# Performance work log

Measured on AMD Instinct MI355X. Metric: run time of the kernel, lower is better.

Reference implementation:

```python
import jax, jax.numpy as jnp
import numpy as np

B, S, D = 4, 1024, 1024
H, HD = 16, 64  # num_heads, head_dim; H*HD == D (qkv_features)
NEG_BIG = -1e10


def setup_inputs() -> dict:
    key = jax.random.key(0)
    ks = jax.random.split(key, 16)
    inp = {
        'inputs_q': jax.random.normal(ks[0], (B, S, D), jnp.float32),
        'inputs_kv': jax.random.normal(ks[1], (B, S, D), jnp.float32),
        'pos_emb_q': jax.random.normal(ks[2], (B, S, D), jnp.float32),
        'pos_emb_k': jax.random.normal(ks[3], (B, S, D), jnp.float32),
        'pos_emb_v': jax.random.normal(ks[4], (B, S, D), jnp.float32),
        'key_padding_mask': jnp.ones((B, S), jnp.float32),
    }
    scale = 1.0 / np.sqrt(D)
    inp['wq'] = jax.random.normal(ks[5], (D, H, HD), jnp.float32) * scale
    inp['bq'] = jnp.zeros((H, HD), jnp.float32)
    inp['wk'] = jax.random.normal(ks[6], (D, H, HD), jnp.float32) * scale
    inp['bk'] = jnp.zeros((H, HD), jnp.float32)
    inp['wv'] = jax.random.normal(ks[7], (D, H, HD), jnp.float32) * scale
    inp['bv'] = jnp.zeros((H, HD), jnp.float32)
    inp['wo'] = jax.random.normal(ks[8], (H, HD, D), jnp.float32) * scale
    inp['bo'] = jnp.zeros((D,), jnp.float32)
    return inp


def reference(inputs_q, inputs_kv, pos_emb_q, pos_emb_k, pos_emb_v,
              key_padding_mask, wq, bq, wk, bk, wv, bv, wo, bo):
    # Add positional embeddings before QKV projections (DETR style).
    q_in = inputs_q + pos_emb_q
    k_in = inputs_kv + pos_emb_k
    v_in = inputs_kv + pos_emb_v
    # DenseGeneral: [b,s,f] x [f,h,d] -> [b,s,h,d]
    q = jnp.einsum('bsf,fhd->bshd', q_in, wq) + bq
    k = jnp.einsum('bsf,fhd->bshd', k_in, wk) + bk
    v = jnp.einsum('bsf,fhd->bshd', v_in, wv) + bv
    # Additive key-padding bias, broadcast to [b,1,1,kv].
    bias = ((1.0 - key_padding_mask) * NEG_BIG)[:, None, None, :]
    q = q / jnp.sqrt(jnp.asarray(HD, q.dtype))
    attn = jnp.einsum('bqhd,bkhd->bhqk', q, k) + bias
    attn = jax.nn.softmax(attn, axis=-1)
    # (train=False: no dropout; identity capture layer is a no-op.)
    x = jnp.einsum('bhqk,bkhd->bqhd', attn, v)
    # Output projection over (heads, head_dim).
    out = jnp.einsum('bqhd,hdf->bqf', x, wo) + bo
    return out
```

## Files before the change

### kernel.cpp

```cpp
#include <hip/hip_runtime.h>
#include <hip/hip_bf16.h>
#include <stdint.h>

typedef __bf16 bf16_t;
typedef __bf16 bf16x8 __attribute__((ext_vector_type(8)));
typedef __bf16 bf16x4v __attribute__((ext_vector_type(4)));
typedef float  f32x4  __attribute__((ext_vector_type(4)));
typedef float  f32x16 __attribute__((ext_vector_type(16)));
typedef unsigned int u32;
typedef u32 u32x4 __attribute__((ext_vector_type(4)));

#define NEG_BIG (-1e10f)
#define LOG2E 1.44269504f

__device__ __forceinline__ void load_lds16(const void* gsrc, void* ldst) {
  __builtin_amdgcn_global_load_lds(
      (__attribute__((address_space(1))) void*)(gsrc),
      (__attribute__((address_space(3))) void*)(ldst), 16, 0, 0);
}

__device__ __forceinline__ u32 cvt_pk_bf16(float lo, float hi) {
  u32 r;
  asm("v_cvt_pk_bf16_f32 %0, %1, %2" : "=v"(r) : "v"(lo), "v"(hi));
  return r;
}

__global__ __launch_bounds__(256) void k_prep_w(
    const float* __restrict__ iq, const float* __restrict__ ikv,
    const float* __restrict__ pq, const float* __restrict__ pk, const float* __restrict__ pv,
    const float* __restrict__ wq, const float* __restrict__ wk,
    const float* __restrict__ wv, const float* __restrict__ wo,
    bf16_t* __restrict__ Xq, bf16_t* __restrict__ Xk, bf16_t* __restrict__ Xv,
    bf16_t* __restrict__ Wt, bf16_t* __restrict__ Wot)
{
  __shared__ float t[64][65];
  if (blockIdx.x < 4096) {
    int i = blockIdx.x * 256 + threadIdx.x;
    float4 a = ((const float4*)iq)[i], b = ((const float4*)ikv)[i];
    float4 eq = ((const float4*)pq)[i], ek = ((const float4*)pk)[i], ev = ((const float4*)pv)[i];
    bf16x4v q, k, v;
    q[0] = (bf16_t)(a.x + eq.x); q[1] = (bf16_t)(a.y + eq.y);
    q[2] = (bf16_t)(a.z + eq.z); q[3] = (bf16_t)(a.w + eq.w);
    k[0] = (bf16_t)(b.x + ek.x); k[1] = (bf16_t)(b.y + ek.y);
    k[2] = (bf16_t)(b.z + ek.z); k[3] = (bf16_t)(b.w + ek.w);
    v[0] = (bf16_t)(b.x + ev.x); v[1] = (bf16_t)(b.y + ev.y);
    v[2] = (bf16_t)(b.z + ev.z); v[3] = (bf16_t)(b.w + ev.w);
    *(bf16x4v*)&Xq[(size_t)i*4] = q;
    *(bf16x4v*)&Xk[(size_t)i*4] = k;
    *(bf16x4v*)&Xv[(size_t)i*4] = v;
  } else {
    int bid = blockIdx.x - 4096;
    int z = bid >> 8, rem = bid & 255;
    const float* src = z==0 ? wq : z==1 ? wk : z==2 ? wv : wo;
    bf16_t*      dst = z < 3 ? (Wt + (size_t)z*(1u<<20)) : Wot;
    int n0 = (rem & 15) << 6, k0 = (rem >> 4) << 6;
    int c = threadIdx.x & 63, rb = threadIdx.x >> 6;
    #pragma unroll
    for (int i = 0; i < 16; ++i) {
      int r = i*4 + rb;
      t[r][c] = src[(size_t)(k0 + r)*1024 + n0 + c];
    }
    __syncthreads();
    #pragma unroll
    for (int i = 0; i < 16; ++i) {
      int r = i*4 + rb;
      dst[(size_t)(n0 + r)*1024 + k0 + c] = (bf16_t)t[c][r];
    }
  }
}

__global__ __launch_bounds__(256, 3) void k_gemm_qkv(
    const bf16_t* __restrict__ Xq, const bf16_t* __restrict__ Xk, const bf16_t* __restrict__ Xv,
    const bf16_t* __restrict__ Wt,
    const float* __restrict__ bq, const float* __restrict__ bk, const float* __restrict__ bv,
    bf16_t* __restrict__ Qo, bf16_t* __restrict__ Ko, bf16_t* __restrict__ Vt)
{
  const int L = blockIdx.x;
  const int w = (L & 7) * 96 + (L >> 3);
  const int bx = w & 7, by = (w >> 3) & 31, bz = w >> 8;
  const int bn = bz * 8 + bx;

  const bf16_t* A = bz==0 ? Xq : bz==1 ? Xk : Xv;
  const float* bias = bz==0 ? bq : bz==1 ? bk : bv;

  __shared__ bf16_t As[128*64];
  __shared__ bf16_t Bs[128*64];

  const int tid = threadIdx.x, lane = tid & 63, wid = tid >> 6;
  const int wm = wid >> 1, wn = wid & 1;
  const int bm0 = by * 128;
  const int bn0g = bn * 128;
  const int g = lane >> 4, c = lane & 15;
  const int sr = lane >> 3, sch = lane & 7;

  f32x4 acc[4][4] = {};

  #define STAGE(kt_)                                                             \
    { _Pragma("unroll")                                                          \
      for (int i = 0; i < 4; ++i) {                                              \
        int r  = wid*32 + i*8 + sr;                                              \
        int ca = sch ^ (r & 7);                                                  \
        load_lds16(A  + (size_t)(bm0  + r)*1024 + (size_t)(kt_)*64 + ca*8,       \
                   &As[(wid*32 + i*8)*64]);                                      \
        load_lds16(Wt + (size_t)(bn0g + r)*1024 + (size_t)(kt_)*64 + ca*8,       \
                   &Bs[(wid*32 + i*8)*64]);                                      \
      } }

  for (int kt = 0; kt < 16; ++kt) {
    STAGE(kt);
    __syncthreads();
    #pragma unroll
    for (int kk = 0; kk < 2; ++kk) {
      bf16x8 af[4], bfr[4];
      #pragma unroll
      for (int m = 0; m < 4; ++m) {
        int row = wm*64 + m*16 + c;
        int ch  = (kk*4 + g) ^ (row & 7);
        af[m] = *(const bf16x8*)&As[row*64 + ch*8];
      }
      #pragma unroll
      for (int n = 0; n < 4; ++n) {
        int row = wn*64 + n*16 + c;
        int ch  = (kk*4 + g) ^ (row & 7);
        bfr[n] = *(const bf16x8*)&Bs[row*64 + ch*8];
      }
      #pragma unroll
      for (int m = 0; m < 4; ++m)
        #pragma unroll
        for (int n = 0; n < 4; ++n)
          acc[m][n] = __builtin_amdgcn_mfma_f32_16x16x32_bf16(af[m], bfr[n], acc[m][n], 0, 0, 0);
    }
    __syncthreads();
  }
  #undef STAGE

  if (bz < 2) {
    bf16_t* C = bz==0 ? Qo : Ko;
    const float scale = bz==0 ? 0.125f * LOG2E : 1.0f;
    #pragma unroll
    for (int n = 0; n < 4; ++n) {
      int col = (bn0g & 1023) + wn*64 + n*16 + c;
      float bn_ = bias[col];
      #pragma unroll
      for (int m = 0; m < 4; ++m) {
        int row0 = bm0 + wm*64 + m*16 + g*4;
        #pragma unroll
        for (int r = 0; r < 4; ++r)
          C[(size_t)(row0 + r)*1024 + col] = (bf16_t)((acc[m][n][r] + bn_) * scale);
      }
    }
  } else {
    #pragma unroll
    for (int n = 0; n < 4; ++n) {
      int colz = (bn0g & 1023) + wn*64 + n*16 + c;
      float bn_ = bias[colz];
      int h = colz >> 6, hd = colz & 63;
      #pragma unroll
      for (int m = 0; m < 4; ++m) {
        int row0 = bm0 + wm*64 + m*16 + g*4;
        int b = row0 >> 10, s0 = row0 & 1023;
        bf16x4v v4;
        #pragma unroll
        for (int r = 0; r < 4; ++r) v4[r] = (bf16_t)(acc[m][n][r] + bn_);
        *(bf16x4v*)&Vt[(size_t)((b*16 + h)*64 + hd)*1024 + s0] = v4;
      }
    }
  }
}

__global__ __launch_bounds__(256, 2) void k_attn2(
    const bf16_t* __restrict__ Qm, const bf16_t* __restrict__ Km,
    const bf16_t* __restrict__ Vt, const float* __restrict__ mask,
    bf16_t* __restrict__ X2)
{
  __shared__ bf16_t Ks[2][64*64];
  __shared__ bf16_t Vs[2][64*64];
  __shared__ float  bias_lds[1024];
  __shared__ int    tflag[16];
  __shared__ float  l_lds[4][32];

  const int L = blockIdx.x;
  const int kk_ = L >> 3;
  const int bh = (L & 7) * 8 + (kk_ >> 3);
  const int qt = kk_ & 7;
  const int b = bh >> 4, h = bh & 15;

  const int tid = threadIdx.x, lane = tid & 63, wid = tid >> 6;
  const int lq = lane & 31;
  const int hi = lane >> 5;

  if (tid < 16) tflag[tid] = 0;
  __syncthreads();
  {
    float4 m4 = *(const float4*)&mask[b*1024 + tid*4];
    float4 b4;
    b4.x = (1.0f - m4.x) * (NEG_BIG * LOG2E);
    b4.y = (1.0f - m4.y) * (NEG_BIG * LOG2E);
    b4.z = (1.0f - m4.z) * (NEG_BIG * LOG2E);
    b4.w = (1.0f - m4.w) * (NEG_BIG * LOG2E);
    *(float4*)&bias_lds[tid*4] = b4;
    if (b4.x != 0.f || b4.y != 0.f || b4.z != 0.f || b4.w != 0.f)
      tflag[tid >> 4] = 1;
  }

  const int q0w = qt*128 + wid*32;
  bf16x8 qf[4];
  #pragma unroll
  for (int kb = 0; kb < 4; ++kb)
    qf[kb] = *(const bf16x8*)&Qm[(size_t)(b*1024 + q0w + lq)*1024 + h*64 + kb*16 + hi*8];

  f32x16 oacc[2] = {};
  float lsum = 0.f;

  const int sr8 = (lane >> 3);
  const int sc8 = lane & 7;
  #define STAGE(bufi, kv0)                                                        \
    {                                                                             \
      _Pragma("unroll")                                                           \
      for (int cc = 0; cc < 2; ++cc) {                                            \
        int r  = cc*32 + wid*8 + sr8;                                             \
        int ca = sc8 ^ (r & 7);                                                   \
        load_lds16(Km + (size_t)(b*1024 + (kv0) + r)*1024 + h*64 + ca*8,          \
                   &Ks[bufi][(cc*32 + wid*8)*64]);                                \
        load_lds16(Vt + (size_t)((b*16 + h)*64 + r)*1024 + (kv0) + ca*8,          \
                   &Vs[bufi][(cc*32 + wid*8)*64]);                                \
      }                                                                           \
    }

  STAGE(0, 0);
  __syncthreads();

  for (int kt = 0; kt < 16; ++kt) {
    const int buf = kt & 1;
    if (kt < 15) STAGE(buf ^ 1, (kt + 1) * 64);

    f32x16 s[2];
    __builtin_amdgcn_s_setprio(1);
    #pragma unroll
    for (int blk = 0; blk < 2; ++blk) {
      f32x16 acc = {};
      #pragma unroll
      for (int kb = 0; kb < 4; ++kb) {
        int row = blk*32 + lq;
        int ch  = (kb*2 + hi) ^ (row & 7);
        bf16x8 kf = *(const bf16x8*)&Ks[buf][row*64 + ch*8];
        acc = __builtin_amdgcn_mfma_f32_32x32x16_bf16(kf, qf[kb], acc, 0, 0, 0);
      }
      s[blk] = acc;
    }
    __builtin_amdgcn_s_setprio(0);

    if (tflag[kt]) {
      #pragma unroll
      for (int blk = 0; blk < 2; ++blk)
        #pragma unroll
        for (int g2 = 0; g2 < 4; ++g2) {
          float4 b4 = *(const float4*)&bias_lds[kt*64 + blk*32 + g2*8 + hi*4];
          s[blk][g2*4+0] += b4.x;
          s[blk][g2*4+1] += b4.y;
          s[blk][g2*4+2] += b4.z;
          s[blk][g2*4+3] += b4.w;
        }
    }

    #pragma unroll
    for (int blk = 0; blk < 2; ++blk)
      #pragma unroll
      for (int r = 0; r < 16; ++r) {
        float sv = fminf(s[blk][r], 60.0f);
        asm("v_exp_f32 %0, %1" : "=v"(sv) : "v"(sv));
        s[blk][r] = sv;
      }

    float ts[8];
    #pragma unroll
    for (int r = 0; r < 8; ++r)
      ts[r] = (s[0][r] + s[0][r+8]) + (s[1][r] + s[1][r+8]);
    float s0 = (ts[0] + ts[1]) + (ts[2] + ts[3]);
    float s1 = (ts[4] + ts[5]) + (ts[6] + ts[7]);
    float rsum = s0 + s1;
    lsum += rsum + __shfl_xor(rsum, 32, 64);

    u32 paw[4][4];
    #pragma unroll
    for (int blk = 0; blk < 2; ++blk)
      #pragma unroll
      for (int half = 0; half < 2; ++half) {
        int base = half * 8;
        #pragma unroll
        for (int w2 = 0; w2 < 2; ++w2) {
          u32 x = cvt_pk_bf16(s[blk][base + 2*w2],     s[blk][base + 2*w2 + 1]);
          u32 y = cvt_pk_bf16(s[blk][base + 4 + 2*w2], s[blk][base + 4 + 2*w2 + 1]);
          asm("v_permlane32_swap_b32 %0, %1" : "+v"(x), "+v"(y));
          paw[blk*2 + half][w2]     = x;
          paw[blk*2 + half][w2 + 2] = y;
        }
      }

    __builtin_amdgcn_s_setprio(1);
    #pragma unroll
    for (int ks = 0; ks < 4; ++ks) {
      u32x4 t = { paw[ks][0], paw[ks][1], paw[ks][2], paw[ks][3] };
      bf16x8 pa = __builtin_bit_cast(bf16x8, t);
      #pragma unroll
      for (int nb = 0; nb < 2; ++nb) {
        int row = nb*32 + lq;
        int ch  = (ks*2 + hi) ^ (row & 7);
        bf16x8 vf = *(const bf16x8*)&Vs[buf][row*64 + ch*8];
        oacc[nb] = __builtin_amdgcn_mfma_f32_32x32x16_bf16(pa, vf, oacc[nb], 0, 0, 0);
      }
    }
    __builtin_amdgcn_s_setprio(0);
    __syncthreads();
  }

  l_lds[wid][lq] = lsum;
  __syncthreads();
  #pragma unroll
  for (int g2 = 0; g2 < 4; ++g2)
    #pragma unroll
    for (int j = 0; j < 4; ++j) {
      int reg  = g2*4 + j;
      int qrow = j + 8*g2 + 4*hi;
      float inv = 1.0f / l_lds[wid][qrow];
      #pragma unroll
      for (int nb = 0; nb < 2; ++nb)
        X2[(size_t)(b*1024 + q0w + qrow)*1024 + h*64 + nb*32 + lq] =
            (bf16_t)(oacc[nb][reg] * inv);
    }
  #undef STAGE
}

__global__ __launch_bounds__(256, 3) void k_gemm_out(
    const bf16_t* __restrict__ A, const bf16_t* __restrict__ Bt,
    const float* __restrict__ bo, float* __restrict__ C)
{
  const int L = blockIdx.x;
  const int w = (L & 7) * 32 + (L >> 3);
  const int bx = w & 7, by = w >> 3;

  __shared__ bf16_t As[128*64];
  __shared__ bf16_t Bs[128*64];

  const int tid = threadIdx.x, lane = tid & 63, wid = tid >> 6;
  const int wm = wid >> 1, wn = wid & 1;
  const int bm0 = by * 128, bn0 = bx * 128;
  const int g = lane >> 4, c = lane & 15;
  const int sr = lane >> 3, sch = lane & 7;

  f32x4 acc[4][4] = {};

  #define STAGEO(kt_)                                                            \
    { _Pragma("unroll")                                                          \
      for (int i = 0; i < 4; ++i) {                                              \
        int r  = wid*32 + i*8 + sr;                                              \
        int ca = sch ^ (r & 7);                                                  \
        load_lds16(A  + (size_t)(bm0 + r)*1024 + (size_t)(kt_)*64 + ca*8,        \
                   &As[(wid*32 + i*8)*64]);                                      \
        load_lds16(Bt + (size_t)(bn0 + r)*1024 + (size_t)(kt_)*64 + ca*8,        \
                   &Bs[(wid*32 + i*8)*64]);                                      \
      } }

  for (int kt = 0; kt < 16; ++kt) {
    STAGEO(kt);
    __syncthreads();
    #pragma unroll
    for (int kk = 0; kk < 2; ++kk) {
      bf16x8 af[4], bfr[4];
      #pragma unroll
      for (int m = 0; m < 4; ++m) {
        int row = wm*64 + m*16 + c;
        int ch  = (kk*4 + g) ^ (row & 7);
        af[m] = *(const bf16x8*)&As[row*64 + ch*8];
      }
      #pragma unroll
      for (int n = 0; n < 4; ++n) {
        int row = wn*64 + n*16 + c;
        int ch  = (kk*4 + g) ^ (row & 7);
        bfr[n] = *(const bf16x8*)&Bs[row*64 + ch*8];
      }
      #pragma unroll
      for (int m = 0; m < 4; ++m)
        #pragma unroll
        for (int n = 0; n < 4; ++n)
          acc[m][n] = __builtin_amdgcn_mfma_f32_16x16x32_bf16(af[m], bfr[n], acc[m][n], 0, 0, 0);
    }
    __syncthreads();
  }
  #undef STAGEO

  #pragma unroll
  for (int n = 0; n < 4; ++n) {
    int col = bn0 + wn*64 + n*16 + c;
    float bn_ = bo[col];
    #pragma unroll
    for (int m = 0; m < 4; ++m) {
      int row0 = bm0 + wm*64 + m*16 + g*4;
      #pragma unroll
      for (int r = 0; r < 4; ++r)
        C[(size_t)(row0 + r)*1024 + col] = acc[m][n][r] + bn_;
    }
  }
}

extern "C" void kernel_launch(void* const* d_in, const int* in_sizes, int n_in,
                              void* d_out, int out_size, void* d_ws, size_t ws_size,
                              hipStream_t stream) {
  const float* iq   = (const float*)d_in[0];
  const float* ikv  = (const float*)d_in[1];
  const float* pq   = (const float*)d_in[2];
  const float* pk   = (const float*)d_in[3];
  const float* pv   = (const float*)d_in[4];
  const float* mask = (const float*)d_in[5];
  const float* wq   = (const float*)d_in[6];
  const float* bq   = (const float*)d_in[7];
  const float* wk   = (const float*)d_in[8];
  const float* bk   = (const float*)d_in[9];
  const float* wv   = (const float*)d_in[10];
  const float* bv   = (const float*)d_in[11];
  const float* wo   = (const float*)d_in[12];
  const float* bo   = (const float*)d_in[13];
  float* out = (float*)d_out;

  char* ws = (char*)d_ws;
  bf16_t* Xq  = (bf16_t*)(ws + (size_t)( 0u<<20));
  bf16_t* Xk  = (bf16_t*)(ws + (size_t)( 8u<<20));
  bf16_t* Xv  = (bf16_t*)(ws + (size_t)(16u<<20));
  bf16_t* Wt  = (bf16_t*)(ws + (size_t)(24u<<20));
  bf16_t* Wot = (bf16_t*)(ws + (size_t)(30u<<20));
  bf16_t* Q   = (bf16_t*)(ws + (size_t)(32u<<20));
  bf16_t* K   = (bf16_t*)(ws + (size_t)(40u<<20));
  bf16_t* Vt  = (bf16_t*)(ws + (size_t)(56u<<20));
  bf16_t* X2  = (bf16_t*)(ws + (size_t)(64u<<20));

  k_prep_w<<<5120, 256, 0, stream>>>(iq, ikv, pq, pk, pv, wq, wk, wv, wo,
                                     Xq, Xk, Xv, Wt, Wot);
  k_gemm_qkv<<<768, 256, 0, stream>>>(Xq, Xk, Xv, Wt, bq, bk, bv, Q, K, Vt);
  k_attn2<<<512, 256, 0, stream>>>(Q, K, Vt, mask, X2);
  k_gemm_out<<<256, 256, 0, stream>>>(X2, Wot, bo, out);
}
```

Baseline: 106.9 us.

## Split attention KV range across two wave groups per block with LDS reduction

The attention kernel now runs 512 threads per block, and two groups of four waves each process half of the key/value sequence for the same query tile. Partial outputs and row sums from the second half are reduced through LDS before normalisation and the store. The goal is more waves per CU and a shorter serial KV loop per wave, so latency is hidden better across the 512 blocks. The cost is doubled LDS for K/V buffers, an extra reduction step with barriers, and possibly lower block occupancy.

```diff
diff --git a/kernel.cpp b/kernel.cpp
--- a/kernel.cpp
+++ b/kernel.cpp
@@ -168,16 +168,17 @@
   }
 }
 
-__global__ __launch_bounds__(256, 2) void k_attn2(
+__global__ __launch_bounds__(512, 4) void k_attn2(
     const bf16_t* __restrict__ Qm, const bf16_t* __restrict__ Km,
     const bf16_t* __restrict__ Vt, const float* __restrict__ mask,
     bf16_t* __restrict__ X2)
 {
-  __shared__ bf16_t Ks[2][64*64];
-  __shared__ bf16_t Vs[2][64*64];
+  __shared__ bf16_t Ks[2][2][64*64];
+  __shared__ bf16_t Vs[2][2][64*64];
   __shared__ float  bias_lds[1024];
   __shared__ int    tflag[16];
   __shared__ float  l_lds[4][32];
+  __shared__ float  l2_lds[4][32];
 
   const int L = blockIdx.x;
   const int kk_ = L >> 3;
@@ -186,24 +187,23 @@
   const int b = bh >> 4, h = bh & 15;
 
   const int tid = threadIdx.x, lane = tid & 63, wid = tid >> 6;
+  const int half = wid >> 2, w4 = wid & 3;
   const int lq = lane & 31;
   const int hi = lane >> 5;
 
   if (tid < 16) tflag[tid] = 0;
   __syncthreads();
   {
-    float4 m4 = *(const float4*)&mask[b*1024 + tid*4];
-    float4 b4;
-    b4.x = (1.0f - m4.x) * (NEG_BIG * LOG2E);
-    b4.y = (1.0f - m4.y) * (NEG_BIG * LOG2E);
-    b4.z = (1.0f - m4.z) * (NEG_BIG * LOG2E);
-    b4.w = (1.0f - m4.w) * (NEG_BIG * LOG2E);
-    *(float4*)&bias_lds[tid*4] = b4;
-    if (b4.x != 0.f || b4.y != 0.f || b4.z != 0.f || b4.w != 0.f)
-      tflag[tid >> 4] = 1;
-  }
-
-  const int q0w = qt*128 + wid*32;
+    float2 m2 = *(const float2*)&mask[b*1024 + tid*2];
+    float2 b2;
+    b2.x = (1.0f - m2.x) * (NEG_BIG * LOG2E);
+    b2.y = (1.0f - m2.y) * (NEG_BIG * LOG2E);
+    *(float2*)&bias_lds[tid*2] = b2;
+    if (b2.x != 0.f || b2.y != 0.f)
+      tflag[tid >> 5] = 1;
+  }
+
+  const int q0w = qt*128 + w4*32;
   bf16x8 qf[4];
   #pragma unroll
   for (int kb = 0; kb < 4; ++kb)
@@ -218,21 +218,22 @@
     {                                                                             \
       _Pragma("unroll")                                                           \
       for (int cc = 0; cc < 2; ++cc) {                                            \
-        int r  = cc*32 + wid*8 + sr8;                                             \
+        int r  = cc*32 + w4*8 + sr8;                                              \
         int ca = sc8 ^ (r & 7);                                                   \
         load_lds16(Km + (size_t)(b*1024 + (kv0) + r)*1024 + h*64 + ca*8,          \
-                   &Ks[bufi][(cc*32 + wid*8)*64]);                                \
+                   &Ks[half][bufi][(cc*32 + w4*8)*64]);                           \
         load_lds16(Vt + (size_t)((b*16 + h)*64 + r)*1024 + (kv0) + ca*8,          \
-                   &Vs[bufi][(cc*32 + wid*8)*64]);                                \
+                   &Vs[half][bufi][(cc*32 + w4*8)*64]);                           \
       }                                                                           \
     }
 
-  STAGE(0, 0);
+  STAGE(0, half*512);
   __syncthreads();
 
-  for (int kt = 0; kt < 16; ++kt) {
-    const int buf = kt & 1;
-    if (kt < 15) STAGE(buf ^ 1, (kt + 1) * 64);
+  for (int t = 0; t < 8; ++t) {
+    const int kt = half*8 + t;
+    const int buf = t & 1;
+    if (t < 7) STAGE(buf ^ 1, (kt + 1) * 64);
 
     f32x16 s[2];
     __builtin_amdgcn_s_setprio(1);
@@ -243,7 +244,7 @@
       for (int kb = 0; kb < 4; ++kb) {
         int row = blk*32 + lq;
         int ch  = (kb*2 + hi) ^ (row & 7);
-        bf16x8 kf = *(const bf16x8*)&Ks[buf][row*64 + ch*8];
+        bf16x8 kf = *(const bf16x8*)&Ks[half][buf][row*64 + ch*8];
         acc = __builtin_amdgcn_mfma_f32_32x32x16_bf16(kf, qf[kb], acc, 0, 0, 0);
       }
       s[blk] = acc;
@@ -285,50 +286,66 @@
     #pragma unroll
     for (int blk = 0; blk < 2; ++blk)
       #pragma unroll
-      for (int half = 0; half < 2; ++half) {
-        int base = half * 8;
+      for (int hf = 0; hf < 2; ++hf) {
+        int base = hf * 8;
         #pragma unroll
         for (int w2 = 0; w2 < 2; ++w2) {
           u32 x = cvt_pk_bf16(s[blk][base + 2*w2],     s[blk][base + 2*w2 + 1]);
           u32 y = cvt_pk_bf16(s[blk][base + 4 + 2*w2], s[blk][base + 4 + 2*w2 + 1]);
           asm("v_permlane32_swap_b32 %0, %1" : "+v"(x), "+v"(y));
-          paw[blk*2 + half][w2]     = x;
-          paw[blk*2 + half][w2 + 2] = y;
+          paw[blk*2 + hf][w2]     = x;
+          paw[blk*2 + hf][w2 + 2] = y;
         }
       }
 
     __builtin_amdgcn_s_setprio(1);
     #pragma unroll
     for (int ks = 0; ks < 4; ++ks) {
-      u32x4 t = { paw[ks][0], paw[ks][1], paw[ks][2], paw[ks][3] };
-      bf16x8 pa = __builtin_bit_cast(bf16x8, t);
+      u32x4 t2 = { paw[ks][0], paw[ks][1], paw[ks][2], paw[ks][3] };
+      bf16x8 pa = __builtin_bit_cast(bf16x8, t2);
       #pragma unroll
       for (int nb = 0; nb < 2; ++nb) {
         int row = nb*32 + lq;
         int ch  = (ks*2 + hi) ^ (row & 7);
-        bf16x8 vf = *(const bf16x8*)&Vs[buf][row*64 + ch*8];
+        bf16x8 vf = *(const bf16x8*)&Vs[half][buf][row*64 + ch*8];
         oacc[nb] = __builtin_amdgcn_mfma_f32_32x32x16_bf16(pa, vf, oacc[nb], 0, 0, 0);
       }
     }
     __builtin_amdgcn_s_setprio(0);
     __syncthreads();
   }
-
-  l_lds[wid][lq] = lsum;
+  #undef STAGE
+
+  float* obuf = (float*)&Vs[0][0][0];
+  if (half == 1) {
+    l2_lds[w4][lq] = lsum;
+    #pragma unroll
+    for (int nb = 0; nb < 2; ++nb)
+      #pragma unroll
+      for (int reg = 0; reg < 16; ++reg)
+        obuf[((((w4*2 + hi)*16 + reg)*2) + nb)*32 + lq] = oacc[nb][reg];
+  }
   __syncthreads();
-  #pragma unroll
-  for (int g2 = 0; g2 < 4; ++g2)
-    #pragma unroll
-    for (int j = 0; j < 4; ++j) {
-      int reg  = g2*4 + j;
-      int qrow = j + 8*g2 + 4*hi;
-      float inv = 1.0f / l_lds[wid][qrow];
-      #pragma unroll
-      for (int nb = 0; nb < 2; ++nb)
-        X2[(size_t)(b*1024 + q0w + qrow)*1024 + h*64 + nb*32 + lq] =
-            (bf16_t)(oacc[nb][reg] * inv);
-    }
-  #undef STAGE
+  if (half == 0) {
+    float lt = lsum + l2_lds[w4][lq];
+    l_lds[w4][lq] = lt;
+  }
+  __syncthreads();
+  if (half == 0) {
+    #pragma unroll
+    for (int g2 = 0; g2 < 4; ++g2)
+      #pragma unroll
+      for (int j = 0; j < 4; ++j) {
+        int reg  = g2*4 + j;
+        int qrow = j + 8*g2 + 4*hi;
+        float inv = 1.0f / l_lds[w4][qrow];
+        #pragma unroll
+        for (int nb = 0; nb < 2; ++nb) {
+          float o = oacc[nb][reg] + obuf[((((w4*2 + hi)*16 + reg)*2) + nb)*32 + lq];
+          X2[(size_t)(b*1024 + q0w + qrow)*1024 + h*64 + nb*32 + lq] = (bf16_t)(o * inv);
+        }
+      }
+  }
 }
 
 __global__ __launch_bounds__(256, 3) void k_gemm_out(
@@ -436,6 +453,6 @@
   k_prep_w<<<5120, 256, 0, stream>>>(iq, ikv, pq, pk, pv, wq, wk, wv, wo,
                                      Xq, Xk, Xv, Wt, Wot);
   k_gemm_qkv<<<768, 256, 0, stream>>>(Xq, Xk, Xv, Wt, bq, bk, bv, Q, K, Vt);
-  k_attn2<<<512, 256, 0, stream>>>(Q, K, Vt, mask, X2);
+  k_attn2<<<512, 512, 0, stream>>>(Q, K, Vt, mask, X2);
   k_gemm_out<<<256, 256, 0, stream>>>(X2, Wot, bo, out);
 }
```

Result: no change. 106.1 us (-0.8%).
